# Optimization experiments

Measured on AMD Instinct MI355X. Metric: run time of the kernel, lower is better.

Reference implementation:

```python
import math
import jax, jax.numpy as jnp
import numpy as np

B, C_IN, C_OUT, D_LATENT, H, W, K = 16, 512, 512, 512, 64, 64, 3
EPS = 1e-8


def setup_inputs() -> dict:
    key = jax.random.key(0)
    ks = jax.random.split(key, 6)
    return {
        "x": jax.random.normal(ks[0], (B, C_IN, H, W), dtype=jnp.float32),
        "w": jax.random.normal(ks[1], (B, D_LATENT), dtype=jnp.float32),
        "noise": jax.random.normal(ks[2], (B, 1, H, W), dtype=jnp.float32),
        "style_w": jax.random.normal(ks[3], (C_IN, D_LATENT), dtype=jnp.float32),
        "style_b": jnp.ones((C_IN,), dtype=jnp.float32),  # bias=1.0 in to_style
        "conv_w": jax.random.normal(ks[4], (C_OUT, C_IN, K, K), dtype=jnp.float32),
        "scale_noise": jax.random.normal(ks[5], (1,), dtype=jnp.float32),
        "bias": jnp.zeros((C_OUT,), dtype=jnp.float32),
    }


def reference(x, w, noise, style_w, style_b, conv_w, scale_noise, bias):
    b, c, h, ww = x.shape
    o, _, k, _ = conv_w.shape
    # EqualizedLinear to_style: runtime_coef = 1/sqrt(d_latent), lr_mul=1
    lin_coef = 1.0 / math.sqrt(style_w.shape[1])
    style = w @ (style_w * lin_coef).T + style_b  # [B, C_in]
    # EqualizedWeight for conv: runtime_coef = 1/sqrt(C_in*K*K)
    conv_coef = 1.0 / math.sqrt(c * k * k)
    weights = (conv_w * conv_coef)[None] * style[:, None, :, None, None]  # [B,O,I,K,K]
    # demodulate
    sigma_inv = jax.lax.rsqrt(jnp.sum(weights * weights, axis=(2, 3, 4), keepdims=True) + EPS)
    weights = weights * sigma_inv
    # grouped conv: groups = batch
    xg = x.reshape(1, b * c, h, ww)
    wg = weights.reshape(b * o, c, k, k)
    y = jax.lax.conv_general_dilated(
        xg, wg, window_strides=(1, 1), padding="SAME",
        feature_group_count=b,
        dimension_numbers=("NCHW", "OIHW", "NCHW"))
    y = y.reshape(b, o, h, ww)
    y = y + scale_noise[None, :, None, None] * noise
    return jax.nn.leaky_relu(y + bias[None, :, None, None], negative_slope=0.2)
```

## Files before the change

kernel.cpp:

```cpp
#include <hip/hip_runtime.h>
#include <hip/hip_bf16.h>


#define B_    16
#define CIN   512
#define COUT  512
#define DLAT  512
#define H_    64
#define W_    64

constexpr float LIN_COEF  = 0.04419417382415922f;
constexpr float CONV_COEF = 0.014731391274719739f;

typedef __attribute__((ext_vector_type(8))) short short8;
typedef __attribute__((ext_vector_type(4))) float f32x4;

__device__ __forceinline__ void gl2lds16(const void* g, void* l) {
  __builtin_amdgcn_global_load_lds(
      (const __attribute__((address_space(1))) unsigned*)g,
      (__attribute__((address_space(3))) unsigned*)l, 16, 0, 0);
}

__global__ __launch_bounds__(256) void pre1(
    const float* __restrict__ w, const float* __restrict__ style_w,
    const float* __restrict__ style_b, const float* __restrict__ conv_w,
    float* __restrict__ style, float* __restrict__ wsq) {
  const int bid = blockIdx.x, tid = threadIdx.x;
  if (bid < 2048) {
    int gw = bid * 4 + (tid >> 6), lane = tid & 63;
    int b = gw >> 9, c = gw & 511;
    const float* wp = w + b * DLAT;
    const float* sw = style_w + c * DLAT;
    float v = 0.f;
    for (int d = lane; d < DLAT; d += 64) v = fmaf(wp[d], sw[d], v);
    #pragma unroll
    for (int off = 32; off > 0; off >>= 1) v += __shfl_down(v, off, 64);
    if (lane == 0) style[b * CIN + c] = fmaf(v, LIN_COEF, style_b[c]);
  } else {
    int idx = (bid - 2048) * 256 + tid;
    const float* p = conv_w + (size_t)idx * 9;
    float s = 0.f;
    #pragma unroll
    for (int t = 0; t < 9; ++t) s = fmaf(p[t], p[t], s);
    wsq[idx] = s;
  }
}

#define LSTR 136
__global__ __launch_bounds__(256) void pre2(
    const float* __restrict__ x, const float* __restrict__ style,
    const float* __restrict__ wsq, const float* __restrict__ conv_w,
    float* __restrict__ scale_bo, __hip_bfloat16* __restrict__ wtp2,
    __hip_bfloat16* __restrict__ xt) {
  __shared__ __align__(16) char sm2[18432];
  const int bid = blockIdx.x, tid = threadIdx.x;
  if (bid < 2048) {
    int gw = bid * 4 + (tid >> 6), lane = tid & 63;
    int b = gw >> 9, o = gw & 511;
    const float* st = style + b * CIN;
    const float* wq = wsq + o * CIN;
    float v = 0.f;
    for (int i = lane; i < CIN; i += 64) { float s = st[i]; v = fmaf(s * s, wq[i], v); }
    #pragma unroll
    for (int off = 32; off > 0; off >>= 1) v += __shfl_down(v, off, 64);
    if (lane == 0)
      scale_bo[b * COUT + o] = CONV_COEF * rsqrtf(fmaf(CONV_COEF * CONV_COEF, v, 1e-8f));
  } else if (bid < 2560) {
    int o = bid - 2048;
    float* lw = (float*)sm2;
    for (int j = tid; j < CIN * 9; j += 256) lw[j] = conv_w[(size_t)o * (CIN * 9) + j];
    __syncthreads();
    for (int g = tid; g < 576; g += 256) {
      int chunk = g / 36, rem = g - chunk * 36, pos = rem >> 2, kqq = rem & 3;
      short8 v;
      #pragma unroll
      for (int e = 0; e < 8; ++e) {
        int ic = chunk * 32 + kqq * 8 + e;
        ((__hip_bfloat16*)&v)[e] = __float2bfloat16(lw[ic * 9 + pos]);
      }
      ((short8*)wtp2)[(size_t)g * 512 + o] = v;
    }
  } else if (bid < 6720) {
    int idx = bid - 2560;
    int b = idx / 260, pb = idx - b * 260;
    int hh, ww;
    if (pb < 66)       { hh = 0;  ww = pb; }
    else if (pb < 132) { hh = 65; ww = pb - 66; }
    else if (pb < 196) { hh = pb - 132 + 1; ww = 0; }
    else               { hh = pb - 196 + 1; ww = 65; }
    unsigned* p = (unsigned*)(xt + (((size_t)b * 66 + hh) * 66 + ww) * CIN);
    p[tid] = 0u;
  } else {
    int idx = bid - 6720;
    int b = idx >> 8, rem = idx & 255, h = rem >> 2, ic0 = (rem & 3) * 128;
    __hip_bfloat16* ls = (__hip_bfloat16*)sm2;
    for (int j = tid; j < 2048; j += 256) {
      int i = j >> 4, wq = j & 15;
      const float4 xv = *(const float4*)&x[(((size_t)b * CIN + ic0 + i) * H_ + h) * W_ + wq * 4];
      float st = style[b * CIN + ic0 + i];
      ls[(wq * 4 + 0) * LSTR + i] = __float2bfloat16(xv.x * st);
      ls[(wq * 4 + 1) * LSTR + i] = __float2bfloat16(xv.y * st);
      ls[(wq * 4 + 2) * LSTR + i] = __float2bfloat16(xv.z * st);
      ls[(wq * 4 + 3) * LSTR + i] = __float2bfloat16(xv.w * st);
    }
    __syncthreads();
    for (int j = tid; j < 1024; j += 256) {
      int ww = j >> 4, part = j & 15;
      __hip_bfloat16* dst = xt + (((size_t)b * 66 + h + 1) * 66 + (ww + 1)) * CIN + ic0 + part * 8;
      *(short8*)dst = *(const short8*)(ls + ww * LSTR + part * 8);
    }
  }
}

__global__ __launch_bounds__(512, 2) void conv_mfma(
    const __hip_bfloat16* __restrict__ xt, const __hip_bfloat16* __restrict__ wtp2,
    const float* __restrict__ scale_bo, const float* __restrict__ noise,
    const float* __restrict__ scale_noise, const float* __restrict__ bias,
    float* __restrict__ out) {
  __shared__ __align__(16) char smem[42240];

  const int tid = threadIdx.x, lane = tid & 63, wv = tid >> 6;
  const int mrow = lane & 15, kq = lane >> 4;
  const int wr = wv >> 1, wc = wv & 1;
  const int b  = blockIdx.x >> 3;
  const int h0 = (blockIdx.x & 7) << 3;
  const int oo0 = (blockIdx.y << 7) + (wc << 6);
  const int r0 = h0 + (wr << 1);

  const size_t xbase = ((size_t)(b * 66 + h0)) * (66 * 512);
  int xoff[6];
  #pragma unroll
  for (int i = 0; i < 6; ++i) {
    int r = i * 64 + lane;
    if (r < 330) {
      int t = wv * 330 + r;
      int p = t >> 2, s = t & 3;
      int q = s ^ ((p >> 1) & 3);
      xoff[i] = p * 512 + q * 8;
    } else xoff[i] = -1;
  }

  f32x4 acc[8][4] = {};
  int pbase[8];
  #pragma unroll
  for (int ms = 0; ms < 8; ++ms)
    pbase[ms] = ((wr << 1) + (ms >> 2)) * 66 + (ms & 3) * 16 + mrow;

  const short8* bbase = (const short8*)wtp2 + (kq * 512 + oo0 + mrow);

  for (int ic0 = 0; ic0 < CIN; ic0 += 32) {
    __syncthreads();
    #pragma unroll
    for (int i = 0; i < 6; ++i)
      if (xoff[i] >= 0)
        gl2lds16(xt + xbase + xoff[i] + ic0, smem + (wv * 330 + i * 64) * 16);
    __syncthreads();

    const int ch9 = (ic0 >> 5) * 9;
    #pragma unroll
    for (int ky = 0; ky < 3; ++ky) {
      #pragma unroll
      for (int kx = 0; kx < 3; ++kx) {
        const short8* bp = bbase + (size_t)(ch9 + ky * 3 + kx) * 2048;
        short8 bf0 = bp[0], bf1 = bp[16], bf2 = bp[32], bf3 = bp[48];
        short8 af[8];
        #pragma unroll
        for (int ms = 0; ms < 8; ++ms) {
          int p = pbase[ms] + ky * 66 + kx;
          int s = kq ^ ((p >> 1) & 3);
          af[ms] = *(const short8*)(smem + p * 64 + s * 16);
        }
        #pragma unroll
        for (int ms = 0; ms < 8; ++ms) {
          acc[ms][0] = __builtin_amdgcn_mfma_f32_16x16x32_bf16(af[ms], bf0, acc[ms][0], 0, 0, 0);
          acc[ms][1] = __builtin_amdgcn_mfma_f32_16x16x32_bf16(af[ms], bf1, acc[ms][1], 0, 0, 0);
          acc[ms][2] = __builtin_amdgcn_mfma_f32_16x16x32_bf16(af[ms], bf2, acc[ms][2], 0, 0, 0);
          acc[ms][3] = __builtin_amdgcn_mfma_f32_16x16x32_bf16(af[ms], bf3, acc[ms][3], 0, 0, 0);
        }
      }
    }
  }

  __syncthreads();
  float* ep = (float*)smem + wv * 1088;
  const float sn = scale_noise[0];

  #pragma unroll
  for (int r = 0; r < 2; ++r) {
    const int h = r0 + r;
    const float nz = sn * noise[((size_t)b * H_ + h) * W_ + lane];
    for (int ns = 0; ns < 4; ++ns) {
      #pragma unroll
      for (int m4 = 0; m4 < 4; ++m4) {
        int ms = r * 4 + m4;
        int prow = m4 * 16 + kq * 4;
        #pragma unroll
        for (int rg = 0; rg < 4; ++rg)
          ep[(prow + rg) * 17 + mrow] = acc[ms][ns][rg];
      }
      #pragma unroll
      for (int oo = 0; oo < 16; ++oo) {
        int o = oo0 + ns * 16 + oo;
        float v = ep[lane * 17 + oo];
        v = fmaf(v, scale_bo[b * COUT + o], nz + bias[o]);
        v = v > 0.f ? v : 0.2f * v;
        out[(((size_t)b * COUT + o) * H_ + h) * W_ + lane] = v;
      }
    }
  }
}

__global__ __launch_bounds__(256) void style_kernel(
    const float* __restrict__ w, const float* __restrict__ style_w,
    const float* __restrict__ style_b, float* __restrict__ style) {
  int gw = blockIdx.x * 4 + (threadIdx.x >> 6);
  int lane = threadIdx.x & 63;
  int b = gw >> 9, c = gw & 511;
  const float* wp = w + b * DLAT;
  const float* sw = style_w + c * DLAT;
  float v = 0.f;
  for (int d = lane; d < DLAT; d += 64) v = fmaf(wp[d], sw[d], v);
  #pragma unroll
  for (int off = 32; off > 0; off >>= 1) v += __shfl_down(v, off, 64);
  if (lane == 0) style[b * CIN + c] = fmaf(v, LIN_COEF, style_b[c]);
}
__global__ __launch_bounds__(256) void wsq_kernel(
    const float* __restrict__ conv_w, float* __restrict__ wsq) {
  int idx = blockIdx.x * 256 + threadIdx.x;
  const float* p = conv_w + (size_t)idx * 9;
  float s = 0.f;
  #pragma unroll
  for (int t = 0; t < 9; ++t) s = fmaf(p[t], p[t], s);
  wsq[idx] = s;
}
__global__ __launch_bounds__(256) void scale_kernel(
    const float* __restrict__ style, const float* __restrict__ wsq,
    float* __restrict__ scale_bo) {
  int gw = blockIdx.x * 4 + (threadIdx.x >> 6);
  int lane = threadIdx.x & 63;
  int b = gw >> 9, o = gw & 511;
  const float* st = style + b * CIN;
  const float* wq = wsq + o * CIN;
  float v = 0.f;
  for (int i = lane; i < CIN; i += 64) { float s = st[i]; v = fmaf(s * s, wq[i], v); }
  #pragma unroll
  for (int off = 32; off > 0; off >>= 1) v += __shfl_down(v, off, 64);
  if (lane == 0)
    scale_bo[b * COUT + o] = CONV_COEF * rsqrtf(fmaf(CONV_COEF * CONV_COEF, v, 1e-8f));
}
#define OTILE 32
#define HTILE 8
#define ICCH  8
#define XSTR  67
#define XROWS 10
__global__ __launch_bounds__(256) void conv_kernel(
    const float* __restrict__ x, const float* __restrict__ style,
    const float* __restrict__ conv_w, const float* __restrict__ scale_bo,
    const float* __restrict__ noise, const float* __restrict__ scale_noise,
    const float* __restrict__ bias, float* __restrict__ out) {
  __shared__ float xtile[ICCH * XROWS * XSTR];
  __shared__ float wt[OTILE * 72];
  const int tid = threadIdx.x;
  const int b = blockIdx.z, o0 = blockIdx.y * OTILE, h0 = blockIdx.x * HTILE;
  const int lane = tid & 63, oq = tid >> 6;
  const int r = lane >> 3, cg = lane & 7;
  float acc[8][8];
  #pragma unroll
  for (int a = 0; a < 8; ++a)
    #pragma unroll
    for (int c = 0; c < 8; ++c) acc[a][c] = 0.f;
  for (int ic0 = 0; ic0 < CIN; ic0 += ICCH) {
    for (int j = tid; j < ICCH * XROWS * XSTR; j += 256) {
      int i = j / (XROWS * XSTR);
      int rem = j - i * (XROWS * XSTR);
      int rr = rem / XSTR, cl = rem - rr * XSTR;
      if (cl < 66) {
        int hh = h0 - 1 + rr, wc = cl - 1;
        float v = 0.f;
        if ((unsigned)hh < 64u && (unsigned)wc < 64u)
          v = x[((size_t)(b * CIN + ic0 + i) * H_ + hh) * W_ + wc] * style[b * CIN + ic0 + i];
        xtile[j] = v;
      }
    }
    for (int j = tid; j < OTILE * 72; j += 256) {
      int oo = j / 72, q = j - oo * 72;
      wt[j] = conv_w[(size_t)(o0 + oo) * (CIN * 9) + ic0 * 9 + q];
    }
    __syncthreads();
    #pragma unroll 1
    for (int i = 0; i < ICCH; ++i) {
      const float* xbi = &xtile[i * (XROWS * XSTR) + r * XSTR + cg * 8];
      const float* wbi = &wt[oq * 8 * 72 + i * 9];
      #pragma unroll
      for (int ky = 0; ky < 3; ++ky) {
        float xr[10];
        #pragma unroll
        for (int q = 0; q < 10; ++q) xr[q] = xbi[ky * XSTR + q];
        #pragma unroll
        for (int kx = 0; kx < 3; ++kx) {
          #pragma unroll
          for (int oo = 0; oo < 8; ++oo) {
            float wv = wbi[oo * 72 + ky * 3 + kx];
            #pragma unroll
            for (int c = 0; c < 8; ++c) acc[oo][c] = fmaf(xr[c + kx], wv, acc[oo][c]);
          }
        }
      }
    }
    __syncthreads();
  }
  const float sn = scale_noise[0];
  const int row = h0 + r;
  float nz[8];
  #pragma unroll
  for (int c = 0; c < 8; ++c)
    nz[c] = sn * noise[((size_t)b * H_ + row) * W_ + cg * 8 + c];
  #pragma unroll
  for (int oo = 0; oo < 8; ++oo) {
    int o = o0 + oq * 8 + oo;
    float s = scale_bo[b * COUT + o];
    float bv = bias[o];
    float* op = out + ((size_t)(b * COUT + o) * H_ + row) * W_ + cg * 8;
    #pragma unroll
    for (int c = 0; c < 8; ++c) {
      float v = fmaf(acc[oo][c], s, nz[c] + bv);
      op[c] = v > 0.f ? v : 0.2f * v;
    }
  }
}

extern "C" void kernel_launch(void* const* d_in, const int* in_sizes, int n_in,
                              void* d_out, int out_size, void* d_ws, size_t ws_size,
                              hipStream_t stream) {
  const float* x           = (const float*)d_in[0];
  const float* w           = (const float*)d_in[1];
  const float* noise       = (const float*)d_in[2];
  const float* style_w     = (const float*)d_in[3];
  const float* style_b     = (const float*)d_in[4];
  const float* conv_w      = (const float*)d_in[5];
  const float* scale_noise = (const float*)d_in[6];
  const float* bias        = (const float*)d_in[7];
  float* out = (float*)d_out;

  float* wsf      = (float*)d_ws;
  float* style    = wsf;
  float* scale_bo = wsf + 8192;
  float* wsq      = wsf + 16384;
  const size_t WTP_OFF = 1114112;
  const size_t XT_OFF  = WTP_OFF + (size_t)COUT * 9 * CIN * 2;
  const size_t NEED    = XT_OFF + (size_t)B_ * 66 * 66 * CIN * 2;

  if (ws_size >= NEED) {
    __hip_bfloat16* wtp2 = (__hip_bfloat16*)((char*)d_ws + WTP_OFF);
    __hip_bfloat16* xtp  = (__hip_bfloat16*)((char*)d_ws + XT_OFF);
    pre1<<<3072, 256, 0, stream>>>(w, style_w, style_b, conv_w, style, wsq);
    pre2<<<10816, 256, 0, stream>>>(x, style, wsq, conv_w, scale_bo, wtp2, xtp);
    dim3 grid(128, 4, 1);
    conv_mfma<<<grid, 512, 0, stream>>>(xtp, wtp2, scale_bo, noise,
                                        scale_noise, bias, out);
  } else {
    style_kernel<<<2048, 256, 0, stream>>>(w, style_w, style_b, style);
    wsq_kernel<<<1024, 256, 0, stream>>>(conv_w, wsq);
    scale_kernel<<<2048, 256, 0, stream>>>(style, wsq, scale_bo);
    dim3 grid(H_ / HTILE, COUT / OTILE, B_);
    conv_kernel<<<grid, 256, 0, stream>>>(x, style, conv_w, scale_bo,
                                          noise, scale_noise, bias, out);
  }
}
```

Before: 494.8 us.

## Stage 64 input channels per barrier pair and remap blocks XCD-aware

The conv kernel now loads two 32-channel slabs into two LDS buffers between each barrier pair, so the number of syncthreads drops by half. The grid is flattened to 512 blocks with a remapping that places the four output-channel quarters of a spatial tile next to each other, likely so blocks on the same XCD share input tiles in L2. LDS use doubles to about 84KB per block, which may cut occupancy from the two blocks per CU the launch bounds request.

```diff
diff --git a/kernel.cpp b/kernel.cpp
--- a/kernel.cpp
+++ b/kernel.cpp
@@ -8,6 +8,9 @@
 #define DLAT  512
 #define H_    64
 #define W_    64
+
+#define ABUF  42240
+#define LDS_BYTES (2 * ABUF)
 
 constexpr float LIN_COEF  = 0.04419417382415922f;
 constexpr float CONV_COEF = 0.014731391274719739f;
@@ -117,15 +120,20 @@
     const float* __restrict__ scale_bo, const float* __restrict__ noise,
     const float* __restrict__ scale_noise, const float* __restrict__ bias,
     float* __restrict__ out) {
-  __shared__ __align__(16) char smem[42240];
+  __shared__ __align__(16) char smem[LDS_BYTES];
 
   const int tid = threadIdx.x, lane = tid & 63, wv = tid >> 6;
   const int mrow = lane & 15, kq = lane >> 4;
   const int wr = wv >> 1, wc = wv & 1;
-  const int b  = blockIdx.x >> 3;
-  const int h0 = (blockIdx.x & 7) << 3;
-  const int oo0 = (blockIdx.y << 7) + (wc << 6);
-  const int r0 = h0 + (wr << 1);
+
+  const int bid = blockIdx.x;
+  const int wg  = (bid & 7) * 64 + (bid >> 3);
+  const int oq  = wg & 3;
+  const int sp  = wg >> 2;
+  const int b   = sp >> 3;
+  const int h0  = (sp & 7) << 3;
+  const int oo0 = (oq << 7) + (wc << 6);
+  const int r0  = h0 + (wr << 1);
 
   const size_t xbase = ((size_t)(b * 66 + h0)) * (66 * 512);
   int xoff[6];
@@ -139,6 +147,7 @@
       xoff[i] = p * 512 + q * 8;
     } else xoff[i] = -1;
   }
+  const int ldst = wv * 5280;
 
   f32x4 acc[8][4] = {};
   int pbase[8];
@@ -148,34 +157,41 @@
 
   const short8* bbase = (const short8*)wtp2 + (kq * 512 + oo0 + mrow);
 
-  for (int ic0 = 0; ic0 < CIN; ic0 += 32) {
+  for (int cc = 0; cc < 8; ++cc) {
+    const int ic0 = cc << 6;
     __syncthreads();
     #pragma unroll
     for (int i = 0; i < 6; ++i)
-      if (xoff[i] >= 0)
-        gl2lds16(xt + xbase + xoff[i] + ic0, smem + (wv * 330 + i * 64) * 16);
-    __syncthreads();
-
-    const int ch9 = (ic0 >> 5) * 9;
-    #pragma unroll
-    for (int ky = 0; ky < 3; ++ky) {
-      #pragma unroll
-      for (int kx = 0; kx < 3; ++kx) {
-        const short8* bp = bbase + (size_t)(ch9 + ky * 3 + kx) * 2048;
-        short8 bf0 = bp[0], bf1 = bp[16], bf2 = bp[32], bf3 = bp[48];
-        short8 af[8];
+      if (xoff[i] >= 0) {
+        gl2lds16(xt + xbase + xoff[i] + ic0,      smem + ldst + i * 1024);
+        gl2lds16(xt + xbase + xoff[i] + ic0 + 32, smem + ABUF + ldst + i * 1024);
+      }
+    __syncthreads();
+
+    #pragma unroll
+    for (int sub = 0; sub < 2; ++sub) {
+      const char* abuf = smem + sub * ABUF;
+      const int ch9 = (cc * 2 + sub) * 9;
+      #pragma unroll
+      for (int ky = 0; ky < 3; ++ky) {
         #pragma unroll
-        for (int ms = 0; ms < 8; ++ms) {
-          int p = pbase[ms] + ky * 66 + kx;
-          int s = kq ^ ((p >> 1) & 3);
-          af[ms] = *(const short8*)(smem + p * 64 + s * 16);
-        }
-        #pragma unroll
-        for (int ms = 0; ms < 8; ++ms) {
-          acc[ms][0] = __builtin_amdgcn_mfma_f32_16x16x32_bf16(af[ms], bf0, acc[ms][0], 0, 0, 0);
-          acc[ms][1] = __builtin_amdgcn_mfma_f32_16x16x32_bf16(af[ms], bf1, acc[ms][1], 0, 0, 0);
-          acc[ms][2] = __builtin_amdgcn_mfma_f32_16x16x32_bf16(af[ms], bf2, acc[ms][2], 0, 0, 0);
-          acc[ms][3] = __builtin_amdgcn_mfma_f32_16x16x32_bf16(af[ms], bf3, acc[ms][3], 0, 0, 0);
+        for (int kx = 0; kx < 3; ++kx) {
+          const short8* bp = bbase + (size_t)(ch9 + ky * 3 + kx) * 2048;
+          short8 bf0 = bp[0], bf1 = bp[16], bf2 = bp[32], bf3 = bp[48];
+          short8 af[8];
+          #pragma unroll
+          for (int ms = 0; ms < 8; ++ms) {
+            int p = pbase[ms] + ky * 66 + kx;
+            int s = kq ^ ((p >> 1) & 3);
+            af[ms] = *(const short8*)(abuf + p * 64 + s * 16);
+          }
+          #pragma unroll
+          for (int ms = 0; ms < 8; ++ms) {
+            acc[ms][0] = __builtin_amdgcn_mfma_f32_16x16x32_bf16(af[ms], bf0, acc[ms][0], 0, 0, 0);
+            acc[ms][1] = __builtin_amdgcn_mfma_f32_16x16x32_bf16(af[ms], bf1, acc[ms][1], 0, 0, 0);
+            acc[ms][2] = __builtin_amdgcn_mfma_f32_16x16x32_bf16(af[ms], bf2, acc[ms][2], 0, 0, 0);
+            acc[ms][3] = __builtin_amdgcn_mfma_f32_16x16x32_bf16(af[ms], bf3, acc[ms][3], 0, 0, 0);
+          }
         }
       }
     }
@@ -355,9 +371,8 @@
     __hip_bfloat16* xtp  = (__hip_bfloat16*)((char*)d_ws + XT_OFF);
     pre1<<<3072, 256, 0, stream>>>(w, style_w, style_b, conv_w, style, wsq);
     pre2<<<10816, 256, 0, stream>>>(x, style, wsq, conv_w, scale_bo, wtp2, xtp);
-    dim3 grid(128, 4, 1);
-    conv_mfma<<<grid, 512, 0, stream>>>(xtp, wtp2, scale_bo, noise,
-                                        scale_noise, bias, out);
+    conv_mfma<<<512, 512, 0, stream>>>(xtp, wtp2, scale_bo, noise,
+                                       scale_noise, bias, out);
   } else {
     style_kernel<<<2048, 256, 0, stream>>>(w, style_w, style_b, style);
     wsq_kernel<<<1024, 256, 0, stream>>>(conv_w, wsq);
```

Result: slower. 682.7 us (+38.0%).
